# Performance work log

Hardware: AMD Instinct MI355X
Metric: run time of the kernel (lower is better)

The kernel has to match this reference:

```python
import jax, jax.numpy as jnp
import numpy as np

N_ENT = 50000
N_REL2 = 100   # num_relations * 2
N_BASES = 16
DIM = 64
N_EDGES = 100000


def _rgcn_conv(x, edge_index, edge_type, edge_norm, basis, att, root, bias):
    # x: [N, D]; basis: [B, D, D]; att: [R, B]; root: [D, D]; bias: [D]
    src = edge_index[0]
    dst = edge_index[1]
    num_nodes = x.shape[0]
    # Per-edge relation weight is w[edge_type] with w = att @ basis (reshaped).
    # By linearity we contract x_j with each basis first, then mix with the
    # per-edge attention coefficients -- same math, avoids the [E, D, D] gather.
    coeff = att[edge_type]                          # [E, B]
    xb = jnp.einsum('ei,bio->ebo', x[src], basis)   # [E, B, D]
    msg = jnp.einsum('eb,ebo->eo', coeff, xb)       # [E, D]
    msg = msg * edge_norm[:, None]
    # scatter-mean aggregation at target nodes
    s = jax.ops.segment_sum(msg, dst, num_segments=num_nodes)
    cnt = jax.ops.segment_sum(jnp.ones((msg.shape[0],), msg.dtype), dst,
                              num_segments=num_nodes)
    agg = s / jnp.maximum(cnt, 1.0)[:, None]
    # root transform + bias
    return agg + x @ root + bias


def setup_inputs() -> dict:
    key = jax.random.key(0)
    ks = jax.random.split(key, 12)
    E = N_EDGES
    inp = {
        'entity': jnp.arange(N_ENT, dtype=jnp.int64) if jax.config.jax_enable_x64 else jnp.arange(N_ENT, dtype=jnp.int32),
        'edge_index': jax.random.randint(ks[0], (2, E), 0, N_ENT),
        'edge_type': jax.random.randint(ks[1], (E,), 0, N_REL2),
        'edge_norm': jax.random.uniform(ks[2], (E,), dtype=jnp.float32),
        'emb': jax.random.normal(ks[3], (N_ENT, DIM), dtype=jnp.float32) * 0.1,
        'basis1': jax.random.normal(ks[4], (N_BASES, DIM, DIM), dtype=jnp.float32) * 0.05,
        'att1': jax.random.normal(ks[5], (N_REL2, N_BASES), dtype=jnp.float32) * 0.1,
        'root1': jax.random.normal(ks[6], (DIM, DIM), dtype=jnp.float32) * 0.05,
        'bias1': jnp.zeros((DIM,), dtype=jnp.float32),
        'basis2': jax.random.normal(ks[7], (N_BASES, DIM, DIM), dtype=jnp.float32) * 0.05,
        'att2': jax.random.normal(ks[8], (N_REL2, N_BASES), dtype=jnp.float32) * 0.1,
        'root2': jax.random.normal(ks[9], (DIM, DIM), dtype=jnp.float32) * 0.05,
        'bias2': jnp.zeros((DIM,), dtype=jnp.float32),
    }
    return inp


def reference(entity, edge_index, edge_type, edge_norm, emb,
              basis1, att1, root1, bias1, basis2, att2, root2, bias2):
    x = emb[entity]                                  # embedding lookup [N, D]
    x = _rgcn_conv(x, edge_index, edge_type, edge_norm, basis1, att1, root1, bias1)
    x = _rgcn_conv(x, edge_index, edge_type, edge_norm, basis2, att2, root2, bias2)
    return x
```

## Files before the change

### kernel.cpp

```cpp
#include <hip/hip_runtime.h>

#define NN 50000
#define NR 100
#define NB 16
#define D  64
#define NE 100000
#define NE2 (NE + 16 * NR)

#define HB  196
#define EPB 512
#define ZB  196
#define GB  ((NN * 16 + 255) / 256)

#define GROUPS 2
#define EPBK (64 * GROUPS)
#define EGRID ((NE2 + EPBK - 1) / EPBK)

#define NPBK 64
#define NGRID ((NN + NPBK - 1) / NPBK)

typedef float f32x4  __attribute__((ext_vector_type(4)));
typedef short bf16x8 __attribute__((ext_vector_type(8)));

__device__ __forceinline__ short f2bf(float f) {
    unsigned u = __float_as_uint(f);
    return (short)((u + 0x7FFFu + ((u >> 16) & 1u)) >> 16);
}

__device__ __forceinline__ bf16x8 pack8(f32x4 a, f32x4 b) {
    bf16x8 t;
    t[0] = f2bf(a.x); t[1] = f2bf(a.y); t[2] = f2bf(a.z); t[3] = f2bf(a.w);
    t[4] = f2bf(b.x); t[5] = f2bf(b.y); t[6] = f2bf(b.z); t[7] = f2bf(b.w);
    return t;
}

__global__ __launch_bounds__(256) void prep_all(
    const float* __restrict__ att1, const float* __restrict__ basis1,
    const float* __restrict__ root1,
    const float* __restrict__ att2, const float* __restrict__ basis2,
    const float* __restrict__ root2,
    const int* __restrict__ entity, const f32x4* __restrict__ emb4,
    float* __restrict__ Wt1, float* __restrict__ Wt2,
    float* __restrict__ rT1, float* __restrict__ rT2,
    f32x4* __restrict__ x04, int* __restrict__ deg, int* __restrict__ nodeCur)
{
    __shared__ float t[64 * 65];
    int b = blockIdx.x;
    if (b < 2 * NR) {
        int layer = b >= NR;
        int r = layer ? b - NR : b;
        const float* att   = layer ? att2 : att1;
        const float* basis = layer ? basis2 : basis1;
        float*       Wt    = layer ? Wt2 : Wt1;
        float a[NB];
#pragma unroll
        for (int bb = 0; bb < NB; ++bb) a[bb] = att[r * NB + bb];
#pragma unroll
        for (int i = 0; i < 16; ++i) {
            int idx = i * 256 + threadIdx.x;
            float acc = 0.f;
#pragma unroll
            for (int bb = 0; bb < NB; ++bb) acc += a[bb] * basis[bb * 4096 + idx];
            t[(idx >> 6) * 65 + (idx & 63)] = acc;
        }
        __syncthreads();
#pragma unroll
        for (int i = 0; i < 16; ++i) {
            int j = i * 256 + threadIdx.x;
            Wt[(size_t)r * 4096 + j] = t[(j & 63) * 65 + (j >> 6)];
        }
    } else if (b < 2 * NR + 2) {
        const float* root = (b == 2 * NR) ? root1 : root2;
        float*       rT   = (b == 2 * NR) ? rT1 : rT2;
#pragma unroll
        for (int i = 0; i < 16; ++i) {
            int idx = i * 256 + threadIdx.x;
            t[(idx >> 6) * 65 + (idx & 63)] = root[idx];
        }
        __syncthreads();
#pragma unroll
        for (int i = 0; i < 16; ++i) {
            int j = i * 256 + threadIdx.x;
            rT[j] = t[(j & 63) * 65 + (j >> 6)];
        }
    } else if (b < 2 * NR + 2 + ZB) {
        int i = (b - (2 * NR + 2)) * 256 + threadIdx.x;
        deg[i] = 0; nodeCur[i] = 0;
    } else {
        int idx = (b - (2 * NR + 2 + ZB)) * 256 + threadIdx.x;
        if (idx < NN * 16) {
            int n = idx >> 4;
            int q = idx & 15;
            x04[idx] = emb4[(size_t)entity[n] * 16 + q];
        }
    }
}

__global__ __launch_bounds__(256) void hist_edges(
    const int* __restrict__ et, const int* __restrict__ dst,
    int* __restrict__ blockHist, int* __restrict__ deg)
{
    __shared__ int lh[NR];
    for (int i = threadIdx.x; i < NR; i += 256) lh[i] = 0;
    __syncthreads();
#pragma unroll
    for (int i = 0; i < EPB / 256; ++i) {
        int e = blockIdx.x * EPB + i * 256 + threadIdx.x;
        if (e < NE) {
            atomicAdd(&lh[et[e]], 1);
            atomicAdd(&deg[dst[e]], 1);
        }
    }
    __syncthreads();
    for (int i = threadIdx.x; i < NR; i += 256)
        blockHist[blockIdx.x * NR + i] = lh[i];
}

__global__ __launch_bounds__(256) void scans(
    const int* __restrict__ blockHist, int* __restrict__ blockPrefix,
    int* __restrict__ relTot, const int* __restrict__ deg,
    int* __restrict__ nodePre, int* __restrict__ blockSumN)
{
    __shared__ int sc[256];
    int t = threadIdx.x;
    if (blockIdx.x < NR) {
        int r = blockIdx.x;
        int v = (t < HB) ? blockHist[t * NR + r] : 0;
        sc[t] = v;
        __syncthreads();
#pragma unroll
        for (int off = 1; off < 256; off <<= 1) {
            int a = (t >= off) ? sc[t - off] : 0;
            __syncthreads();
            sc[t] += a;
            __syncthreads();
        }
        if (t < HB) blockPrefix[t * NR + r] = sc[t] - v;
        if (t == 0) relTot[r] = sc[255];
    } else {
        int b = blockIdx.x - NR;
        int n = b * 256 + t;
        int v = deg[n];
        sc[t] = v;
        __syncthreads();
#pragma unroll
        for (int off = 1; off < 256; off <<= 1) {
            int a = (t >= off) ? sc[t - off] : 0;
            __syncthreads();
            sc[t] += a;
            __syncthreads();
        }
        nodePre[n] = sc[t] - v;
        if (t == 255) blockSumN[b] = sc[255];
    }
}

__global__ __launch_bounds__(256) void scanK(
    const int* __restrict__ relTot, const int* __restrict__ blockSumN,
    int* __restrict__ offs, int* __restrict__ nbG, int* __restrict__ nodeBB,
    int* __restrict__ srcS, float* __restrict__ normS, int* __restrict__ rS)
{
    __shared__ int totL[NR];
    __shared__ int offL[NR + 1];
    __shared__ int sc2[256];
    int t = threadIdx.x;
    if (t < NR) totL[t] = relTot[t];
    int v2 = (t < ZB) ? blockSumN[t] : 0;
    sc2[t] = v2;
    __syncthreads();
    if (t == 0) {
        int off = 0;
        for (int r = 0; r < NR; ++r) {
            offL[r] = off;
            off = (off + totL[r] + 15) & ~15;
        }
        offL[NR] = off;
    }
    __syncthreads();
#pragma unroll
    for (int off = 1; off < 256; off <<= 1) {
        int a = (t >= off) ? sc2[t - off] : 0;
        __syncthreads();
        sc2[t] += a;
        __syncthreads();
    }
    if (t < ZB) nodeBB[t] = sc2[t] - v2;
    if (t == 0) nodeBB[ZB] = sc2[255];
    if (t <= NR) offs[t] = offL[t];
    if (t == 0) nbG[0] = offL[NR];
    if (t < NR) {
        int g0 = offL[t] + totL[t], g1 = offL[t + 1];
        for (int p = g0; p < g1; ++p) { srcS[p] = 0; normS[p] = 0.f; rS[p] = t; }
    }
}

__global__ __launch_bounds__(256) void scatter2(
    const int* __restrict__ src, const int* __restrict__ dst,
    const int* __restrict__ et, const float* __restrict__ en,
    const int* __restrict__ offs, const int* __restrict__ blockPrefix,
    const int* __restrict__ nodePre, const int* __restrict__ nodeBlockBase,
    int* __restrict__ nodeCur, int* __restrict__ srcS,
    float* __restrict__ normS, int* __restrict__ rS, int* __restrict__ dstIdx)
{
    __shared__ int lcur[NR];
    for (int i = threadIdx.x; i < NR; i += 256)
        lcur[i] = offs[i] + blockPrefix[blockIdx.x * NR + i];
    __syncthreads();
#pragma unroll
    for (int i = 0; i < EPB / 256; ++i) {
        int e = blockIdx.x * EPB + i * 256 + threadIdx.x;
        if (e < NE) {
            int r = et[e];
            int p = atomicAdd(&lcur[r], 1);
            srcS[p] = src[e]; normS[p] = en[e]; rS[p] = r;
            int n = dst[e];
            int q = nodeBlockBase[n >> 8] + nodePre[n] + atomicAdd(&nodeCur[n], 1);
            dstIdx[q] = p;
        }
    }
}

__global__ __launch_bounds__(256) void edge_mfma(
    const int* __restrict__ srcS, const float* __restrict__ normS,
    const int* __restrict__ rS, const int* __restrict__ nbG,
    const float* __restrict__ x, const float* __restrict__ Wt,
    float* __restrict__ msg)
{
    int tid = threadIdx.x;
    int lane = tid & 63, wid = tid >> 6;
    int c15 = lane & 15, kg = lane >> 4;
    int padTot = nbG[0];
    int rcur = -1;
    bf16x8 B[4][2];

#pragma unroll 1
    for (int g = 0; g < GROUPS; ++g) {
        int gs = blockIdx.x * EPBK + wid * (16 * GROUPS) + g * 16;
        if (gs >= padTot) break;
        int r = __builtin_amdgcn_readfirstlane(rS[gs]);
        if (r != rcur) {
            rcur = r;
            const float* __restrict__ Wr = Wt + (size_t)r * 4096;
#pragma unroll
            for (int nt = 0; nt < 4; ++nt)
#pragma unroll
                for (int ks = 0; ks < 2; ++ks) {
                    const f32x4* p = (const f32x4*)(Wr + (nt * 16 + c15) * 64 + ks * 32 + kg * 8);
                    B[nt][ks] = pack8(p[0], p[1]);
                }
        }
        int e  = gs + c15;
        float nrm = normS[e];
        int   sn  = srcS[e];
        const f32x4* xr  = (const f32x4*)(x + (size_t)sn * 64 + kg * 8);
        const f32x4* xr2 = (const f32x4*)(x + (size_t)sn * 64 + 32 + kg * 8);
        bf16x8 A0 = pack8(xr[0]  * nrm, xr[1]  * nrm);
        bf16x8 A1 = pack8(xr2[0] * nrm, xr2[1] * nrm);

        f32x4 z = {0.f, 0.f, 0.f, 0.f};
        f32x4 acc[4] = {z, z, z, z};
#pragma unroll
        for (int nt = 0; nt < 4; ++nt) {
            acc[nt] = __builtin_amdgcn_mfma_f32_16x16x32_bf16(A0, B[nt][0], acc[nt], 0, 0, 0);
            acc[nt] = __builtin_amdgcn_mfma_f32_16x16x32_bf16(A1, B[nt][1], acc[nt], 0, 0, 0);
        }
#pragma unroll
        for (int nt = 0; nt < 4; ++nt)
#pragma unroll
            for (int j = 0; j < 4; ++j)
                msg[(size_t)(gs + kg * 4 + j) * 64 + nt * 16 + c15] = acc[nt][j];
    }
}

__global__ __launch_bounds__(256) void agg_node(
    const float* __restrict__ x, const float* __restrict__ msg,
    const int* __restrict__ dstIdx, const int* __restrict__ nodePre,
    const int* __restrict__ nodeBB, const float* __restrict__ rT,
    const float* __restrict__ bias, float* __restrict__ agg,
    float* __restrict__ out)
{
    int tid = threadIdx.x;
    int lane = tid & 63, wid = tid >> 6;
    int c15 = lane & 15, kg = lane >> 4;
    int wbase = blockIdx.x * NPBK + wid * 16;

#pragma unroll 1
    for (int ln = 0; ln < 16; ++ln) {
        int n = wbase + ln;
        if (n >= NN) break;
        int blk  = n >> 8;
        int base = nodeBB[blk];
        int lo = base + nodePre[n];
        int hi = ((n & 255) == 255) ? nodeBB[blk + 1] : base + nodePre[n + 1];
        float acc = 0.f;
        for (int q = lo; q < hi; ++q)
            acc += msg[(size_t)dstIdx[q] * 64 + lane];
        float c = (float)(hi - lo);
        c = c > 1.f ? c : 1.f;
        agg[(size_t)n * 64 + lane] = acc / c;
    }
    __syncthreads();

    if (wbase >= NN) return;
    int ge = wbase + 16 < NN ? wbase + 16 : NN;

    bf16x8 B[4][2];
#pragma unroll
    for (int nt = 0; nt < 4; ++nt)
#pragma unroll
        for (int ks = 0; ks < 2; ++ks) {
            const f32x4* p = (const f32x4*)(rT + (nt * 16 + c15) * 64 + ks * 32 + kg * 8);
            B[nt][ks] = pack8(p[0], p[1]);
        }
    float bv[4];
#pragma unroll
    for (int nt = 0; nt < 4; ++nt) bv[nt] = bias[nt * 16 + c15];

    int n  = wbase + c15;
    int nc = n < ge ? n : ge - 1;
    const f32x4* xr  = (const f32x4*)(x + (size_t)nc * 64 + kg * 8);
    const f32x4* xr2 = (const f32x4*)(x + (size_t)nc * 64 + 32 + kg * 8);
    bf16x8 A0 = pack8(xr[0], xr[1]);
    bf16x8 A1 = pack8(xr2[0], xr2[1]);

    f32x4 z = {0.f, 0.f, 0.f, 0.f};
    f32x4 acc[4] = {z, z, z, z};
#pragma unroll
    for (int nt = 0; nt < 4; ++nt) {
        acc[nt] = __builtin_amdgcn_mfma_f32_16x16x32_bf16(A0, B[nt][0], acc[nt], 0, 0, 0);
        acc[nt] = __builtin_amdgcn_mfma_f32_16x16x32_bf16(A1, B[nt][1], acc[nt], 0, 0, 0);
    }
#pragma unroll
    for (int nt = 0; nt < 4; ++nt)
#pragma unroll
        for (int j = 0; j < 4; ++j) {
            int nr = wbase + kg * 4 + j;
            if (nr < ge) {
                size_t off = (size_t)nr * 64 + nt * 16 + c15;
                out[off] = agg[off] + acc[nt][j] + bv[nt];
            }
        }
}

extern "C" void kernel_launch(void* const* d_in, const int* in_sizes, int n_in,
                              void* d_out, int out_size, void* d_ws, size_t ws_size,
                              hipStream_t stream) {
    const int*   entity    = (const int*)d_in[0];
    const int*   edge_index= (const int*)d_in[1];
    const int*   edge_type = (const int*)d_in[2];
    const float* edge_norm = (const float*)d_in[3];
    const float* emb       = (const float*)d_in[4];
    const float* basis1    = (const float*)d_in[5];
    const float* att1      = (const float*)d_in[6];
    const float* root1     = (const float*)d_in[7];
    const float* bias1     = (const float*)d_in[8];
    const float* basis2    = (const float*)d_in[9];
    const float* att2      = (const float*)d_in[10];
    const float* root2     = (const float*)d_in[11];
    const float* bias2     = (const float*)d_in[12];

    const int* src = edge_index;
    const int* dst = edge_index + NE;

    float* ws    = (float*)d_ws;
    float* Wt1   = ws;
    float* Wt2   = Wt1 + (size_t)NR * 4096;
    float* rT1   = Wt2 + (size_t)NR * 4096;
    float* rT2   = rT1 + 4096;
    float* x0    = rT2 + 4096;
    float* msg   = x0  + (size_t)NN * D;
    float* agg   = msg + (size_t)NE2 * D;
    float* normS = agg + (size_t)NN * D;
    int*   offs        = (int*)(normS + NE2);
    int*   relTot      = offs + NR + 3;
    int*   nbG         = relTot + NR;
    int*   blockHist   = nbG + 3;
    int*   blockPrefix = blockHist + HB * NR;
    int*   srcS        = blockPrefix + HB * NR;
    int*   rS          = srcS + NE2;
    int*   deg         = rS + NE2;
    int*   nodePre     = deg + ZB * 256;
    int*   nodeCur     = nodePre + ZB * 256;
    int*   blockSumN   = nodeCur + ZB * 256;
    int*   nodeBB      = blockSumN + ZB + 4;
    int*   dstIdx      = nodeBB + ZB + 5;

    float* out = (float*)d_out;

    prep_all<<<2 * NR + 2 + ZB + GB, 256, 0, stream>>>(
        att1, basis1, root1, att2, basis2, root2,
        entity, (const f32x4*)emb, Wt1, Wt2, rT1, rT2,
        (f32x4*)x0, deg, nodeCur);
    hist_edges<<<HB, 256, 0, stream>>>(edge_type, dst, blockHist, deg);
    scans<<<NR + ZB, 256, 0, stream>>>(blockHist, blockPrefix, relTot,
                                       deg, nodePre, blockSumN);
    scanK<<<1, 256, 0, stream>>>(relTot, blockSumN, offs, nbG, nodeBB,
                                 srcS, normS, rS);
    scatter2<<<HB, 256, 0, stream>>>(src, dst, edge_type, edge_norm,
                                     offs, blockPrefix, nodePre, nodeBB,
                                     nodeCur, srcS, normS, rS, dstIdx);

    edge_mfma<<<EGRID, 256, 0, stream>>>(srcS, normS, rS, nbG, x0, Wt1, msg);
    agg_node<<<NGRID, 256, 0, stream>>>(x0, msg, dstIdx, nodePre, nodeBB,
                                        rT1, bias1, agg, out);

    edge_mfma<<<EGRID, 256, 0, stream>>>(srcS, normS, rS, nbG, out, Wt2, msg);
    agg_node<<<NGRID, 256, 0, stream>>>(out, msg, dstIdx, nodePre, nodeBB,
                                        rT2, bias2, agg, out);
}
```

Baseline: 155.9 us.

## Scatter edge messages into destination-sorted order and split aggregation from root transform

Edge messages are now written straight to their destination-sorted slot through a per-edge position map (qOf), so aggregation reads contiguous rows instead of gathering through dstIdx. Padding edges are mapped to spare slots past NE. The fused agg_node kernel is split into agg_mean, with one wavefront per node and many more blocks, and node_mfma, with 128 nodes per block. This removes the indirect gather and the serial 16-node loop per wave, but it adds one kernel launch per layer and makes the msg stores scattered.

```diff
diff --git a/kernel.cpp b/kernel.cpp
--- a/kernel.cpp
+++ b/kernel.cpp
@@ -16,7 +16,7 @@
 #define EPBK (64 * GROUPS)
 #define EGRID ((NE2 + EPBK - 1) / EPBK)
 
-#define NPBK 64
+#define NPBK 128
 #define NGRID ((NN + NPBK - 1) / NPBK)
 
 typedef float f32x4  __attribute__((ext_vector_type(4)));
@@ -158,10 +158,12 @@
 __global__ __launch_bounds__(256) void scanK(
     const int* __restrict__ relTot, const int* __restrict__ blockSumN,
     int* __restrict__ offs, int* __restrict__ nbG, int* __restrict__ nodeBB,
-    int* __restrict__ srcS, float* __restrict__ normS, int* __restrict__ rS)
+    int* __restrict__ srcS, float* __restrict__ normS, int* __restrict__ rS,
+    int* __restrict__ qOf)
 {
     __shared__ int totL[NR];
     __shared__ int offL[NR + 1];
+    __shared__ int gapB[NR];
     __shared__ int sc2[256];
     int t = threadIdx.x;
     if (t < NR) totL[t] = relTot[t];
@@ -169,10 +171,12 @@
     sc2[t] = v2;
     __syncthreads();
     if (t == 0) {
-        int off = 0;
+        int off = 0, real = 0;
         for (int r = 0; r < NR; ++r) {
             offL[r] = off;
+            gapB[r] = off - real;
             off = (off + totL[r] + 15) & ~15;
+            real += totL[r];
         }
         offL[NR] = off;
     }
@@ -190,7 +194,10 @@
     if (t == 0) nbG[0] = offL[NR];
     if (t < NR) {
         int g0 = offL[t] + totL[t], g1 = offL[t + 1];
-        for (int p = g0; p < g1; ++p) { srcS[p] = 0; normS[p] = 0.f; rS[p] = t; }
+        for (int p = g0; p < g1; ++p) {
+            srcS[p] = 0; normS[p] = 0.f; rS[p] = t;
+            qOf[p] = NE + gapB[t] + (p - g0);
+        }
     }
 }
 
@@ -200,7 +207,7 @@
     const int* __restrict__ offs, const int* __restrict__ blockPrefix,
     const int* __restrict__ nodePre, const int* __restrict__ nodeBlockBase,
     int* __restrict__ nodeCur, int* __restrict__ srcS,
-    float* __restrict__ normS, int* __restrict__ rS, int* __restrict__ dstIdx)
+    float* __restrict__ normS, int* __restrict__ rS, int* __restrict__ qOf)
 {
     __shared__ int lcur[NR];
     for (int i = threadIdx.x; i < NR; i += 256)
@@ -214,17 +221,16 @@
             int p = atomicAdd(&lcur[r], 1);
             srcS[p] = src[e]; normS[p] = en[e]; rS[p] = r;
             int n = dst[e];
-            int q = nodeBlockBase[n >> 8] + nodePre[n] + atomicAdd(&nodeCur[n], 1);
-            dstIdx[q] = p;
+            qOf[p] = nodeBlockBase[n >> 8] + nodePre[n] + atomicAdd(&nodeCur[n], 1);
         }
     }
 }
 
 __global__ __launch_bounds__(256) void edge_mfma(
     const int* __restrict__ srcS, const float* __restrict__ normS,
-    const int* __restrict__ rS, const int* __restrict__ nbG,
-    const float* __restrict__ x, const float* __restrict__ Wt,
-    float* __restrict__ msg)
+    const int* __restrict__ rS, const int* __restrict__ qOf,
+    const int* __restrict__ nbG, const float* __restrict__ x,
+    const float* __restrict__ Wt, float* __restrict__ msg)
 {
     int tid = threadIdx.x;
     int lane = tid & 63, wid = tid >> 6;
@@ -249,6 +255,11 @@
                     B[nt][ks] = pack8(p[0], p[1]);
                 }
         }
+        int q0 = qOf[gs + kg * 4 + 0];
+        int q1 = qOf[gs + kg * 4 + 1];
+        int q2 = qOf[gs + kg * 4 + 2];
+        int q3 = qOf[gs + kg * 4 + 3];
+
         int e  = gs + c15;
         float nrm = normS[e];
         int   sn  = srcS[e];
@@ -264,45 +275,42 @@
             acc[nt] = __builtin_amdgcn_mfma_f32_16x16x32_bf16(A0, B[nt][0], acc[nt], 0, 0, 0);
             acc[nt] = __builtin_amdgcn_mfma_f32_16x16x32_bf16(A1, B[nt][1], acc[nt], 0, 0, 0);
         }
+        int qv[4] = {q0, q1, q2, q3};
 #pragma unroll
         for (int nt = 0; nt < 4; ++nt)
 #pragma unroll
             for (int j = 0; j < 4; ++j)
-                msg[(size_t)(gs + kg * 4 + j) * 64 + nt * 16 + c15] = acc[nt][j];
-    }
-}
-
-__global__ __launch_bounds__(256) void agg_node(
-    const float* __restrict__ x, const float* __restrict__ msg,
-    const int* __restrict__ dstIdx, const int* __restrict__ nodePre,
-    const int* __restrict__ nodeBB, const float* __restrict__ rT,
-    const float* __restrict__ bias, float* __restrict__ agg,
+                msg[(size_t)qv[j] * 64 + nt * 16 + c15] = acc[nt][j];
+    }
+}
+
+__global__ __launch_bounds__(256) void agg_mean(
+    const float* __restrict__ msg, const int* __restrict__ nodePre,
+    const int* __restrict__ nodeBB, float* __restrict__ agg)
+{
+    int n    = blockIdx.x * 4 + (threadIdx.x >> 6);
+    int lane = threadIdx.x & 63;
+    if (n >= NN) return;
+    int blk  = n >> 8;
+    int base = nodeBB[blk];
+    int lo = base + nodePre[n];
+    int hi = ((n & 255) == 255) ? nodeBB[blk + 1] : base + nodePre[n + 1];
+    float acc = 0.f;
+    for (int q = lo; q < hi; ++q)
+        acc += msg[(size_t)q * 64 + lane];
+    float c = (float)(hi - lo);
+    c = c > 1.f ? c : 1.f;
+    agg[(size_t)n * 64 + lane] = acc / c;
+}
+
+__global__ __launch_bounds__(256) void node_mfma(
+    const float* __restrict__ x, const float* __restrict__ agg,
+    const float* __restrict__ rT, const float* __restrict__ bias,
     float* __restrict__ out)
 {
     int tid = threadIdx.x;
     int lane = tid & 63, wid = tid >> 6;
     int c15 = lane & 15, kg = lane >> 4;
-    int wbase = blockIdx.x * NPBK + wid * 16;
-
-#pragma unroll 1
-    for (int ln = 0; ln < 16; ++ln) {
-        int n = wbase + ln;
-        if (n >= NN) break;
-        int blk  = n >> 8;
-        int base = nodeBB[blk];
-        int lo = base + nodePre[n];
-        int hi = ((n & 255) == 255) ? nodeBB[blk + 1] : base + nodePre[n + 1];
-        float acc = 0.f;
-        for (int q = lo; q < hi; ++q)
-            acc += msg[(size_t)dstIdx[q] * 64 + lane];
-        float c = (float)(hi - lo);
-        c = c > 1.f ? c : 1.f;
-        agg[(size_t)n * 64 + lane] = acc / c;
-    }
-    __syncthreads();
-
-    if (wbase >= NN) return;
-    int ge = wbase + 16 < NN ? wbase + 16 : NN;
 
     bf16x8 B[4][2];
 #pragma unroll
@@ -316,30 +324,37 @@
 #pragma unroll
     for (int nt = 0; nt < 4; ++nt) bv[nt] = bias[nt * 16 + c15];
 
-    int n  = wbase + c15;
-    int nc = n < ge ? n : ge - 1;
-    const f32x4* xr  = (const f32x4*)(x + (size_t)nc * 64 + kg * 8);
-    const f32x4* xr2 = (const f32x4*)(x + (size_t)nc * 64 + 32 + kg * 8);
-    bf16x8 A0 = pack8(xr[0], xr[1]);
-    bf16x8 A1 = pack8(xr2[0], xr2[1]);
-
-    f32x4 z = {0.f, 0.f, 0.f, 0.f};
-    f32x4 acc[4] = {z, z, z, z};
-#pragma unroll
-    for (int nt = 0; nt < 4; ++nt) {
-        acc[nt] = __builtin_amdgcn_mfma_f32_16x16x32_bf16(A0, B[nt][0], acc[nt], 0, 0, 0);
-        acc[nt] = __builtin_amdgcn_mfma_f32_16x16x32_bf16(A1, B[nt][1], acc[nt], 0, 0, 0);
-    }
-#pragma unroll
-    for (int nt = 0; nt < 4; ++nt)
-#pragma unroll
-        for (int j = 0; j < 4; ++j) {
-            int nr = wbase + kg * 4 + j;
-            if (nr < ge) {
-                size_t off = (size_t)nr * 64 + nt * 16 + c15;
-                out[off] = agg[off] + acc[nt][j] + bv[nt];
+#pragma unroll 1
+    for (int g = 0; g < 2; ++g) {
+        int gs = blockIdx.x * NPBK + wid * 32 + g * 16;
+        if (gs >= NN) break;
+        int ge = gs + 16 < NN ? gs + 16 : NN;
+
+        int n  = gs + c15;
+        int nc = n < ge ? n : ge - 1;
+        const f32x4* xr  = (const f32x4*)(x + (size_t)nc * 64 + kg * 8);
+        const f32x4* xr2 = (const f32x4*)(x + (size_t)nc * 64 + 32 + kg * 8);
+        bf16x8 A0 = pack8(xr[0], xr[1]);
+        bf16x8 A1 = pack8(xr2[0], xr2[1]);
+
+        f32x4 z = {0.f, 0.f, 0.f, 0.f};
+        f32x4 acc[4] = {z, z, z, z};
+#pragma unroll
+        for (int nt = 0; nt < 4; ++nt) {
+            acc[nt] = __builtin_amdgcn_mfma_f32_16x16x32_bf16(A0, B[nt][0], acc[nt], 0, 0, 0);
+            acc[nt] = __builtin_amdgcn_mfma_f32_16x16x32_bf16(A1, B[nt][1], acc[nt], 0, 0, 0);
+        }
+#pragma unroll
+        for (int nt = 0; nt < 4; ++nt)
+#pragma unroll
+            for (int j = 0; j < 4; ++j) {
+                int nr = gs + kg * 4 + j;
+                if (nr < ge) {
+                    size_t off = (size_t)nr * 64 + nt * 16 + c15;
+                    out[off] = agg[off] + acc[nt][j] + bv[nt];
+                }
             }
-        }
+    }
 }
 
 extern "C" void kernel_launch(void* const* d_in, const int* in_sizes, int n_in,
@@ -378,12 +393,12 @@
     int*   blockPrefix = blockHist + HB * NR;
     int*   srcS        = blockPrefix + HB * NR;
     int*   rS          = srcS + NE2;
-    int*   deg         = rS + NE2;
+    int*   qOf         = rS + NE2;
+    int*   deg         = qOf + NE2;
     int*   nodePre     = deg + ZB * 256;
     int*   nodeCur     = nodePre + ZB * 256;
     int*   blockSumN   = nodeCur + ZB * 256;
     int*   nodeBB      = blockSumN + ZB + 4;
-    int*   dstIdx      = nodeBB + ZB + 5;
 
     float* out = (float*)d_out;
 
@@ -395,16 +410,16 @@
     scans<<<NR + ZB, 256, 0, stream>>>(blockHist, blockPrefix, relTot,
                                        deg, nodePre, blockSumN);
     scanK<<<1, 256, 0, stream>>>(relTot, blockSumN, offs, nbG, nodeBB,
-                                 srcS, normS, rS);
+                                 srcS, normS, rS, qOf);
     scatter2<<<HB, 256, 0, stream>>>(src, dst, edge_type, edge_norm,
                                      offs, blockPrefix, nodePre, nodeBB,
-                                     nodeCur, srcS, normS, rS, dstIdx);
-
-    edge_mfma<<<EGRID, 256, 0, stream>>>(srcS, normS, rS, nbG, x0, Wt1, msg);
-    agg_node<<<NGRID, 256, 0, stream>>>(x0, msg, dstIdx, nodePre, nodeBB,
-                                        rT1, bias1, agg, out);
-
-    edge_mfma<<<EGRID, 256, 0, stream>>>(srcS, normS, rS, nbG, out, Wt2, msg);
-    agg_node<<<NGRID, 256, 0, stream>>>(out, msg, dstIdx, nodePre, nodeBB,
-                                        rT2, bias2, agg, out);
-}
+                                     nodeCur, srcS, normS, rS, qOf);
+
+    edge_mfma<<<EGRID, 256, 0, stream>>>(srcS, normS, rS, qOf, nbG, x0, Wt1, msg);
+    agg_mean<<<(NN + 3) / 4, 256, 0, stream>>>(msg, nodePre, nodeBB, agg);
+    node_mfma<<<NGRID, 256, 0, stream>>>(x0, agg, rT1, bias1, out);
+
+    edge_mfma<<<EGRID, 256, 0, stream>>>(srcS, normS, rS, qOf, nbG, out, Wt2, msg);
+    agg_mean<<<(NN + 3) / 4, 256, 0, stream>>>(msg, nodePre, nodeBB, agg);
+    node_mfma<<<NGRID, 256, 0, stream>>>(out, agg, rT2, bias2, out);
+}
```

New measurement: 133.5 us. 14.4% less time.

## Keep per-node aggregates in LDS and shrink agg_node blocks to 16 nodes

Applied to the files above, without the earlier changes.

agg_node now handles 16 nodes per block instead of 64. Each of the four waves gathers four nodes and writes the mean into a shared-memory tile rather than a global agg buffer, and wave 0 then does the root MFMA and reads the aggregate from LDS. This removes a global write and read of the N×64 aggregate buffer and launches four times more blocks, spreading the gather better. In exchange, three of the four waves sit idle during the MFMA epilogue, and the bounds checks are dropped because NN is divisible by 16.

```diff
diff --git a/kernel.cpp b/kernel.cpp
--- a/kernel.cpp
+++ b/kernel.cpp
@@ -16,8 +16,7 @@
 #define EPBK (64 * GROUPS)
 #define EGRID ((NE2 + EPBK - 1) / EPBK)
 
-#define NPBK 64
-#define NGRID ((NN + NPBK - 1) / NPBK)
+#define NAB (NN / 16)
 
 typedef float f32x4  __attribute__((ext_vector_type(4)));
 typedef short bf16x8 __attribute__((ext_vector_type(8)));
@@ -272,22 +271,21 @@
     }
 }
 
-__global__ __launch_bounds__(256) void agg_node(
+__global__ __launch_bounds__(256, 4) void agg_node(
     const float* __restrict__ x, const float* __restrict__ msg,
     const int* __restrict__ dstIdx, const int* __restrict__ nodePre,
     const int* __restrict__ nodeBB, const float* __restrict__ rT,
-    const float* __restrict__ bias, float* __restrict__ agg,
-    float* __restrict__ out)
-{
+    const float* __restrict__ bias, float* __restrict__ out)
+{
+    __shared__ float aggL[16][68];
     int tid = threadIdx.x;
     int lane = tid & 63, wid = tid >> 6;
-    int c15 = lane & 15, kg = lane >> 4;
-    int wbase = blockIdx.x * NPBK + wid * 16;
+    int nb = blockIdx.x * 16;
 
 #pragma unroll 1
-    for (int ln = 0; ln < 16; ++ln) {
-        int n = wbase + ln;
-        if (n >= NN) break;
+    for (int i = 0; i < 4; ++i) {
+        int ln = wid * 4 + i;
+        int n = nb + ln;
         int blk  = n >> 8;
         int base = nodeBB[blk];
         int lo = base + nodePre[n];
@@ -297,13 +295,12 @@
             acc += msg[(size_t)dstIdx[q] * 64 + lane];
         float c = (float)(hi - lo);
         c = c > 1.f ? c : 1.f;
-        agg[(size_t)n * 64 + lane] = acc / c;
-    }
-    __syncthreads();
-
-    if (wbase >= NN) return;
-    int ge = wbase + 16 < NN ? wbase + 16 : NN;
-
+        aggL[ln][lane] = acc / c;
+    }
+    __syncthreads();
+    if (wid != 0) return;
+
+    int c15 = lane & 15, kg = lane >> 4;
     bf16x8 B[4][2];
 #pragma unroll
     for (int nt = 0; nt < 4; ++nt)
@@ -316,10 +313,9 @@
 #pragma unroll
     for (int nt = 0; nt < 4; ++nt) bv[nt] = bias[nt * 16 + c15];
 
-    int n  = wbase + c15;
-    int nc = n < ge ? n : ge - 1;
-    const f32x4* xr  = (const f32x4*)(x + (size_t)nc * 64 + kg * 8);
-    const f32x4* xr2 = (const f32x4*)(x + (size_t)nc * 64 + 32 + kg * 8);
+    int n = nb + c15;
+    const f32x4* xr  = (const f32x4*)(x + (size_t)n * 64 + kg * 8);
+    const f32x4* xr2 = (const f32x4*)(x + (size_t)n * 64 + 32 + kg * 8);
     bf16x8 A0 = pack8(xr[0], xr[1]);
     bf16x8 A1 = pack8(xr2[0], xr2[1]);
 
@@ -334,11 +330,9 @@
     for (int nt = 0; nt < 4; ++nt)
 #pragma unroll
         for (int j = 0; j < 4; ++j) {
-            int nr = wbase + kg * 4 + j;
-            if (nr < ge) {
-                size_t off = (size_t)nr * 64 + nt * 16 + c15;
-                out[off] = agg[off] + acc[nt][j] + bv[nt];
-            }
+            int nr = nb + kg * 4 + j;
+            out[(size_t)nr * 64 + nt * 16 + c15] =
+                aggL[kg * 4 + j][nt * 16 + c15] + acc[nt][j] + bv[nt];
         }
 }
 
@@ -369,8 +363,7 @@
     float* rT2   = rT1 + 4096;
     float* x0    = rT2 + 4096;
     float* msg   = x0  + (size_t)NN * D;
-    float* agg   = msg + (size_t)NE2 * D;
-    float* normS = agg + (size_t)NN * D;
+    float* normS = msg + (size_t)NE2 * D;
     int*   offs        = (int*)(normS + NE2);
     int*   relTot      = offs + NR + 3;
     int*   nbG         = relTot + NR;
@@ -401,10 +394,10 @@
                                      nodeCur, srcS, normS, rS, dstIdx);
 
     edge_mfma<<<EGRID, 256, 0, stream>>>(srcS, normS, rS, nbG, x0, Wt1, msg);
-    agg_node<<<NGRID, 256, 0, stream>>>(x0, msg, dstIdx, nodePre, nodeBB,
-                                        rT1, bias1, agg, out);
+    agg_node<<<NAB, 256, 0, stream>>>(x0, msg, dstIdx, nodePre, nodeBB,
+                                      rT1, bias1, out);
 
     edge_mfma<<<EGRID, 256, 0, stream>>>(srcS, normS, rS, nbG, out, Wt2, msg);
-    agg_node<<<NGRID, 256, 0, stream>>>(out, msg, dstIdx, nodePre, nodeBB,
-                                        rT2, bias2, agg, out);
-}
+    agg_node<<<NAB, 256, 0, stream>>>(out, msg, dstIdx, nodePre, nodeBB,
+                                      rT2, bias2, out);
+}
```

After: 137.7 us. 11.7% less time.

## Store edge messages in bf16 and split aggregation from root-transform MFMA

Applied to the files above, without the earlier changes.

Edge messages are now written as bf16 rather than fp32, which halves the traffic for the message write and for the gather. The fused agg_node kernel is split into agg_mean, with one wave per node and a wide grid for more parallel gather, and node_mfma, where each wave handles two 16-node groups with NPBK set to 128. This costs an extra kernel launch per layer and a round trip of the agg buffer through memory, and adds bf16 rounding error to the messages.

```diff
diff --git a/kernel.cpp b/kernel.cpp
--- a/kernel.cpp
+++ b/kernel.cpp
@@ -16,15 +16,20 @@
 #define EPBK (64 * GROUPS)
 #define EGRID ((NE2 + EPBK - 1) / EPBK)
 
-#define NPBK 64
+#define NPBK 128
 #define NGRID ((NN + NPBK - 1) / NPBK)
 
 typedef float f32x4  __attribute__((ext_vector_type(4)));
 typedef short bf16x8 __attribute__((ext_vector_type(8)));
+typedef unsigned short u16;
 
 __device__ __forceinline__ short f2bf(float f) {
     unsigned u = __float_as_uint(f);
     return (short)((u + 0x7FFFu + ((u >> 16) & 1u)) >> 16);
+}
+
+__device__ __forceinline__ float bf2f(u16 u) {
+    return __uint_as_float((unsigned)u << 16);
 }
 
 __device__ __forceinline__ bf16x8 pack8(f32x4 a, f32x4 b) {
@@ -224,7 +229,7 @@
     const int* __restrict__ srcS, const float* __restrict__ normS,
     const int* __restrict__ rS, const int* __restrict__ nbG,
     const float* __restrict__ x, const float* __restrict__ Wt,
-    float* __restrict__ msg)
+    u16* __restrict__ msg)
 {
     int tid = threadIdx.x;
     int lane = tid & 63, wid = tid >> 6;
@@ -268,41 +273,39 @@
         for (int nt = 0; nt < 4; ++nt)
 #pragma unroll
             for (int j = 0; j < 4; ++j)
-                msg[(size_t)(gs + kg * 4 + j) * 64 + nt * 16 + c15] = acc[nt][j];
-    }
-}
-
-__global__ __launch_bounds__(256) void agg_node(
-    const float* __restrict__ x, const float* __restrict__ msg,
-    const int* __restrict__ dstIdx, const int* __restrict__ nodePre,
-    const int* __restrict__ nodeBB, const float* __restrict__ rT,
-    const float* __restrict__ bias, float* __restrict__ agg,
+                msg[(size_t)(gs + kg * 4 + j) * 64 + nt * 16 + c15] =
+                    (u16)f2bf(acc[nt][j]);
+    }
+}
+
+__global__ __launch_bounds__(256) void agg_mean(
+    const u16* __restrict__ msg, const int* __restrict__ dstIdx,
+    const int* __restrict__ nodePre, const int* __restrict__ nodeBB,
+    float* __restrict__ agg)
+{
+    int n    = blockIdx.x * 4 + (threadIdx.x >> 6);
+    int lane = threadIdx.x & 63;
+    if (n >= NN) return;
+    int blk  = n >> 8;
+    int base = nodeBB[blk];
+    int lo = base + nodePre[n];
+    int hi = ((n & 255) == 255) ? nodeBB[blk + 1] : base + nodePre[n + 1];
+    float acc = 0.f;
+    for (int q = lo; q < hi; ++q)
+        acc += bf2f(msg[(size_t)dstIdx[q] * 64 + lane]);
+    float c = (float)(hi - lo);
+    c = c > 1.f ? c : 1.f;
+    agg[(size_t)n * 64 + lane] = acc / c;
+}
+
+__global__ __launch_bounds__(256) void node_mfma(
+    const float* __restrict__ x, const float* __restrict__ agg,
+    const float* __restrict__ rT, const float* __restrict__ bias,
     float* __restrict__ out)
 {
     int tid = threadIdx.x;
     int lane = tid & 63, wid = tid >> 6;
     int c15 = lane & 15, kg = lane >> 4;
-    int wbase = blockIdx.x * NPBK + wid * 16;
-
-#pragma unroll 1
-    for (int ln = 0; ln < 16; ++ln) {
-        int n = wbase + ln;
-        if (n >= NN) break;
-        int blk  = n >> 8;
-        int base = nodeBB[blk];
-        int lo = base + nodePre[n];
-        int hi = ((n & 255) == 255) ? nodeBB[blk + 1] : base + nodePre[n + 1];
-        float acc = 0.f;
-        for (int q = lo; q < hi; ++q)
-            acc += msg[(size_t)dstIdx[q] * 64 + lane];
-        float c = (float)(hi - lo);
-        c = c > 1.f ? c : 1.f;
-        agg[(size_t)n * 64 + lane] = acc / c;
-    }
-    __syncthreads();
-
-    if (wbase >= NN) return;
-    int ge = wbase + 16 < NN ? wbase + 16 : NN;
 
     bf16x8 B[4][2];
 #pragma unroll
@@ -316,30 +319,37 @@
 #pragma unroll
     for (int nt = 0; nt < 4; ++nt) bv[nt] = bias[nt * 16 + c15];
 
-    int n  = wbase + c15;
-    int nc = n < ge ? n : ge - 1;
-    const f32x4* xr  = (const f32x4*)(x + (size_t)nc * 64 + kg * 8);
-    const f32x4* xr2 = (const f32x4*)(x + (size_t)nc * 64 + 32 + kg * 8);
-    bf16x8 A0 = pack8(xr[0], xr[1]);
-    bf16x8 A1 = pack8(xr2[0], xr2[1]);
-
-    f32x4 z = {0.f, 0.f, 0.f, 0.f};
-    f32x4 acc[4] = {z, z, z, z};
-#pragma unroll
-    for (int nt = 0; nt < 4; ++nt) {
-        acc[nt] = __builtin_amdgcn_mfma_f32_16x16x32_bf16(A0, B[nt][0], acc[nt], 0, 0, 0);
-        acc[nt] = __builtin_amdgcn_mfma_f32_16x16x32_bf16(A1, B[nt][1], acc[nt], 0, 0, 0);
-    }
-#pragma unroll
-    for (int nt = 0; nt < 4; ++nt)
-#pragma unroll
-        for (int j = 0; j < 4; ++j) {
-            int nr = wbase + kg * 4 + j;
-            if (nr < ge) {
-                size_t off = (size_t)nr * 64 + nt * 16 + c15;
-                out[off] = agg[off] + acc[nt][j] + bv[nt];
+#pragma unroll 1
+    for (int g = 0; g < 2; ++g) {
+        int gs = blockIdx.x * NPBK + wid * 32 + g * 16;
+        if (gs >= NN) break;
+        int ge = gs + 16 < NN ? gs + 16 : NN;
+
+        int n  = gs + c15;
+        int nc = n < ge ? n : ge - 1;
+        const f32x4* xr  = (const f32x4*)(x + (size_t)nc * 64 + kg * 8);
+        const f32x4* xr2 = (const f32x4*)(x + (size_t)nc * 64 + 32 + kg * 8);
+        bf16x8 A0 = pack8(xr[0], xr[1]);
+        bf16x8 A1 = pack8(xr2[0], xr2[1]);
+
+        f32x4 z = {0.f, 0.f, 0.f, 0.f};
+        f32x4 acc[4] = {z, z, z, z};
+#pragma unroll
+        for (int nt = 0; nt < 4; ++nt) {
+            acc[nt] = __builtin_amdgcn_mfma_f32_16x16x32_bf16(A0, B[nt][0], acc[nt], 0, 0, 0);
+            acc[nt] = __builtin_amdgcn_mfma_f32_16x16x32_bf16(A1, B[nt][1], acc[nt], 0, 0, 0);
+        }
+#pragma unroll
+        for (int nt = 0; nt < 4; ++nt)
+#pragma unroll
+            for (int j = 0; j < 4; ++j) {
+                int nr = gs + kg * 4 + j;
+                if (nr < ge) {
+                    size_t off = (size_t)nr * 64 + nt * 16 + c15;
+                    out[off] = agg[off] + acc[nt][j] + bv[nt];
+                }
             }
-        }
+    }
 }
 
 extern "C" void kernel_launch(void* const* d_in, const int* in_sizes, int n_in,
@@ -368,10 +378,10 @@
     float* rT1   = Wt2 + (size_t)NR * 4096;
     float* rT2   = rT1 + 4096;
     float* x0    = rT2 + 4096;
-    float* msg   = x0  + (size_t)NN * D;
-    float* agg   = msg + (size_t)NE2 * D;
+    float* agg   = x0  + (size_t)NN * D;
     float* normS = agg + (size_t)NN * D;
-    int*   offs        = (int*)(normS + NE2);
+    u16*   msg   = (u16*)(normS + NE2);
+    int*   offs        = (int*)(msg + (size_t)NE2 * D);
     int*   relTot      = offs + NR + 3;
     int*   nbG         = relTot + NR;
     int*   blockHist   = nbG + 3;
@@ -401,10 +411,10 @@
                                      nodeCur, srcS, normS, rS, dstIdx);
 
     edge_mfma<<<EGRID, 256, 0, stream>>>(srcS, normS, rS, nbG, x0, Wt1, msg);
-    agg_node<<<NGRID, 256, 0, stream>>>(x0, msg, dstIdx, nodePre, nodeBB,
-                                        rT1, bias1, agg, out);
+    agg_mean<<<(NN + 3) / 4, 256, 0, stream>>>(msg, dstIdx, nodePre, nodeBB, agg);
+    node_mfma<<<NGRID, 256, 0, stream>>>(x0, agg, rT1, bias1, out);
 
     edge_mfma<<<EGRID, 256, 0, stream>>>(srcS, normS, rS, nbG, out, Wt2, msg);
-    agg_node<<<NGRID, 256, 0, stream>>>(out, msg, dstIdx, nodePre, nodeBB,
-                                        rT2, bias2, agg, out);
-}
+    agg_mean<<<(NN + 3) / 4, 256, 0, stream>>>(msg, dstIdx, nodePre, nodeBB, agg);
+    node_mfma<<<NGRID, 256, 0, stream>>>(out, agg, rT2, bias2, out);
+}
```

After: 136.7 us. -12.3%, faster.
